# Optimization experiments

Hardware: AMD Instinct MI355X
Metric: run time of the kernel (lower is better)

The kernel has to match this reference:

```python
import jax, jax.numpy as jnp
import numpy as np

CLASSES = 128
H = 448  # half_height
W = 608  # half_width
B = 1
E = CLASSES * H  # 57344 experts
SCALE = 0.02


def setup_inputs() -> dict:
    key = jax.random.key(0)
    ks = jax.random.split(key, 10)
    return {
        "x": jax.random.normal(ks[0], (B, 128, H, W), jnp.float32),
        "x_gt": jax.random.uniform(ks[1], (B, 1, H, W), jnp.float32),
        # grouped 1x1 router conv (groups=H): per-row linear 128 -> CLASSES
        "Wc": jax.random.normal(ks[2], (H, CLASSES, 128), jnp.float32) * SCALE,
        "bc": jax.random.normal(ks[3], (H, CLASSES), jnp.float32) * SCALE,
        # CondMul expert tables: weight [E, in, out], bias [E, out]
        "W1": jax.random.normal(ks[4], (E, 128, 32), jnp.float32) * SCALE,
        "b1": jax.random.normal(ks[5], (E, 32), jnp.float32) * SCALE,
        "W2": jax.random.normal(ks[6], (E, 32, 32), jnp.float32) * SCALE,
        "b2": jax.random.normal(ks[7], (E, 32), jnp.float32) * SCALE,
        "Wrc": jax.random.normal(ks[8], (E, 32, 2), jnp.float32) * SCALE,
        "brc": jax.random.normal(ks[9], (E, 2), jnp.float32) * SCALE,
    }


def cond_mul(xf, flat_inds, Wt, bt):
    """Per-row expert matmul: y[n] = xf[n] @ Wt[flat_inds[n]] + bt[flat_inds[n]].
    Chunked with lax.map to avoid materializing the full [N, in, out] gather."""
    n, cin = xf.shape
    cout = Wt.shape[-1]
    nch = H  # N = B*H*W, chunk by row -> each chunk gathers [B*W, cin, cout]
    xs = xf.reshape(nch, -1, cin)
    idx = flat_inds.reshape(nch, -1)
    def f(args):
        xc, ic = args
        return jnp.einsum('ni,nio->no', xc, Wt[ic]) + bt[ic]
    return jax.lax.map(f, (xs, idx)).reshape(n, cout)


def reference(x, x_gt, Wc, bc, W1, b1, W2, b2, Wrc, brc):
    lrelu = jax.nn.leaky_relu  # negative_slope=0.01 (torch default)
    # --- router: grouped 1x1 conv == per-height-row linear 128 -> CLASSES ---
    xr = jnp.transpose(x, (0, 2, 1, 3))  # [B, H, 128, W]
    logits = jnp.einsum('bhiw,hci->bhcw', xr, Wc) + bc[None, :, :, None]
    logits = lrelu(logits)  # [B, H, C, W]
    # training path (x_gt given): softmax then cross_entropy (as in source)
    probs = jax.nn.softmax(jnp.transpose(logits, (0, 2, 1, 3)), axis=1)  # [B, C, H, W]
    inds = jnp.clip((x_gt * CLASSES).astype(jnp.int32), 0, CLASSES - 1)  # [B, 1, H, W]
    labels = inds[:, 0]  # [B, H, W]
    lsm = jax.nn.log_softmax(probs, axis=1)
    loss_class = -jnp.take_along_axis(lsm, labels[:, None], axis=1)[:, 0]  # [B, H, W]
    # --- expert index: class + row*CLASSES ---
    offset = jnp.arange(H, dtype=jnp.int32)[None, None, :, None]
    flat_inds = (inds + offset * CLASSES).reshape(-1)  # [B*H*W]
    # --- chained CondMul experts: 128 -> 32 -> 32 -> 2, fused leaky_relu ---
    xf = jnp.transpose(x, (0, 2, 3, 1)).reshape(-1, 128)  # [B*H*W, 128]
    h = lrelu(cond_mul(xf, flat_inds, W1, b1))
    h = lrelu(cond_mul(h, flat_inds, W2, b2))
    h = lrelu(cond_mul(h, flat_inds, Wrc, brc))
    out = jnp.transpose(h.reshape(B, H, W, 2), (0, 3, 1, 2))  # [B, 2, H, W]
    mask = out[:, 1]
    reg = out[:, 0]
    # calc_x_pos (broadcast [B,1,H,W] + [B,H,W] as in torch; exact for B=1)
    x_pos = inds.astype(jnp.float32) * (1.0 / CLASSES) + reg * (1.0 / CLASSES)
    return x_pos, mask, loss_class
```

## Files before the change

### kernel.cpp

```cpp
#include <hip/hip_runtime.h>
#include <hip/hip_bf16.h>

#define HH 448
#define WW 608
#define CC 128
#define HWP (HH*WW)
#define G 8

typedef __attribute__((ext_vector_type(8))) short bf16x8;
typedef __attribute__((ext_vector_type(4))) float f32x4;

__device__ __forceinline__ ushort f2b(float f) {
    __hip_bfloat16 b = __float2bfloat16(f);
    return *reinterpret_cast<ushort*>(&b);
}
__device__ __forceinline__ float b2f(ushort u) {
    union { unsigned v; float f; } x; x.v = ((unsigned)u) << 16; return x.f;
}
__device__ __forceinline__ float lrelu(float a) { return a > 0.f ? a : 0.01f * a; }

__device__ __forceinline__ int swzA(int m, int k) {
    return m * 128 + ((((k >> 3) ^ (m & 15)) & 15) << 3) + (k & 7);
}
__device__ __forceinline__ int swzB(int n, int k) {
    return n * 64 + ((((k >> 3) ^ (n & 7) ^ ((n >> 3) & 7)) & 7) << 3) + (k & 7);
}

__global__ __launch_bounds__(512, 4) void k1_mfma(
    const float* __restrict__ x, const float* __restrict__ x_gt,
    const float* __restrict__ Wc, const float* __restrict__ bc,
    float* __restrict__ loss_out, int* __restrict__ labels,
    ushort* __restrict__ xT, int use_xT)
{
    __shared__ ushort Wcs[128 * 128];
    __shared__ ushort Xs[128 * 64];
    __shared__ float bcs[128];

    const int h  = blockIdx.y;
    const int w0 = blockIdx.x * 128;
    const int t  = threadIdx.x;
    const int wv = t >> 6, l = t & 63;
    const int q  = l >> 4, lm = l & 15;
    const int nvalid = (WW - w0 < 128) ? (WW - w0) : 128;

    const float* Wch = Wc + (size_t)h * (CC * 128);
    #pragma unroll
    for (int it = 0; it < 8; ++it) {
        int f4 = t + (it << 9);
        float4 v = reinterpret_cast<const float4*>(Wch)[f4];
        int e = f4 << 2; int m = e >> 7, kk = e & 127;
        ushort4 u = make_ushort4(f2b(v.x), f2b(v.y), f2b(v.z), f2b(v.w));
        *reinterpret_cast<ushort4*>(&Wcs[swzA(m, kk)]) = u;
    }
    if (t < 128) bcs[t] = bc[h * CC + t];

    f32x4 acc[8];
    #pragma unroll
    for (int mt = 0; mt < 8; ++mt) acc[mt] = (f32x4){0.f, 0.f, 0.f, 0.f};

    for (int kh = 0; kh < 2; ++kh) {
        if (kh) __syncthreads();
        #pragma unroll
        for (int it = 0; it < 2; ++it) {
            int p = t + (it << 9);
            int i2 = p >> 5;
            int w = (p & 31) << 2;
            float4 v0, v1;
            if (w0 + w < WW) {
                const float* xb = x + ((size_t)(kh * 64 + i2 * 2)) * HWP + (size_t)h * WW + w0 + w;
                v0 = *reinterpret_cast<const float4*>(xb);
                v1 = *reinterpret_cast<const float4*>(xb + HWP);
            } else { v0 = make_float4(0, 0, 0, 0); v1 = v0; }
            int il = i2 << 1;
            *reinterpret_cast<ushort2*>(&Xs[swzB(w + 0, il)]) = make_ushort2(f2b(v0.x), f2b(v1.x));
            *reinterpret_cast<ushort2*>(&Xs[swzB(w + 1, il)]) = make_ushort2(f2b(v0.y), f2b(v1.y));
            *reinterpret_cast<ushort2*>(&Xs[swzB(w + 2, il)]) = make_ushort2(f2b(v0.z), f2b(v1.z));
            *reinterpret_cast<ushort2*>(&Xs[swzB(w + 3, il)]) = make_ushort2(f2b(v0.w), f2b(v1.w));
        }
        __syncthreads();

        #pragma unroll
        for (int kk = 0; kk < 2; ++kk) {
            const int kb = (kk << 5) + (q << 3);
            const int kg = (kh << 6) + kb;
            bf16x8 bfrag = *reinterpret_cast<const bf16x8*>(&Xs[swzB((wv << 4) + lm, kb)]);
            #pragma unroll
            for (int mt = 0; mt < 8; ++mt) {
                bf16x8 afrag = *reinterpret_cast<const bf16x8*>(&Wcs[swzA((mt << 4) + lm, kg)]);
                acc[mt] = __builtin_amdgcn_mfma_f32_16x16x32_bf16(afrag, bfrag, acc[mt], 0, 0, 0);
            }
        }

        if (use_xT) {
            #pragma unroll
            for (int it = 0; it < 2; ++it) {
                int g = t + (it << 9);
                int n = g >> 3, i8 = g & 7;
                if (n < nvalid) {
                    bf16x8 v = *reinterpret_cast<const bf16x8*>(&Xs[swzB(n, i8 << 3)]);
                    *reinterpret_cast<bf16x8*>(xT + ((size_t)(h * WW + w0 + n)) * 128 + (kh << 6) + (i8 << 3)) = v;
                }
            }
        }
    }

    const int cn = (wv << 4) + lm;
    const int w  = w0 + cn;
    float mx = -1e30f;
    #pragma unroll
    for (int mt = 0; mt < 8; ++mt)
        #pragma unroll
        for (int r = 0; r < 4; ++r) {
            float z = acc[mt][r] + bcs[(mt << 4) + (q << 2) + r];
            z = z > 0.f ? z : 0.01f * z;
            acc[mt][r] = z;
            mx = fmaxf(mx, z);
        }
    mx = fmaxf(mx, __shfl_xor(mx, 16));
    mx = fmaxf(mx, __shfl_xor(mx, 32));
    float s1 = 0.f;
    #pragma unroll
    for (int mt = 0; mt < 8; ++mt)
        #pragma unroll
        for (int r = 0; r < 4; ++r) {
            float ev = __expf(acc[mt][r] - mx);
            acc[mt][r] = ev;
            s1 += ev;
        }
    s1 += __shfl_xor(s1, 16);
    s1 += __shfl_xor(s1, 32);
    const float inv = 1.f / s1;
    float s2 = 0.f;
    #pragma unroll
    for (int mt = 0; mt < 8; ++mt)
        #pragma unroll
        for (int r = 0; r < 4; ++r) s2 += __expf(acc[mt][r] * inv);
    s2 += __shfl_xor(s2, 16);
    s2 += __shfl_xor(s2, 32);

    int lab = 0;
    if (w < WW) {
        float g = x_gt[(size_t)h * WW + w];
        lab = (int)(g * 128.f);
        lab = lab < 0 ? 0 : (lab > 127 ? 127 : lab);
    }
    float pl = 0.f;
    #pragma unroll
    for (int mt = 0; mt < 8; ++mt)
        #pragma unroll
        for (int r = 0; r < 4; ++r)
            if (((mt << 4) + (q << 2) + r) == lab) pl = acc[mt][r] * inv;
    pl += __shfl_xor(pl, 16);
    pl += __shfl_xor(pl, 32);

    if (q == 0 && w < WW) {
        loss_out[(size_t)h * WW + w] = __logf(s2) - pl;
        labels[h * WW + w] = lab;
    }
}

__global__ __launch_bounds__(256, 2) void k2_mfma(
    const float* __restrict__ x, const ushort* __restrict__ xT, int use_xT,
    const int* __restrict__ labels,
    const float* __restrict__ W1, const float* __restrict__ b1,
    const float* __restrict__ W2, const float* __restrict__ b2,
    const float* __restrict__ Wrc, const float* __restrict__ brc,
    float* __restrict__ out)
{
    __shared__ ushort wlist[WW];
    __shared__ int cnt8[G], off8[G], cur8[G];
    __shared__ ushort __align__(16) hA[4][16][40];
    __shared__ float h2s[4][16][33];
    __shared__ float wrcs[4][64];

    const int cg = blockIdx.x, h = blockIdx.y;
    const int c0 = cg * G;
    const size_t E0 = (size_t)h * CC + c0;
    const int t = threadIdx.x;
    const int wv = t >> 6, l = t & 63;
    const int lo = l & 15, g = l >> 4;

    if (t < G) { cnt8[t] = 0; cur8[t] = 0; }
    __syncthreads();

    const int* lrow = labels + h * WW;
    int myl[3];
    #pragma unroll
    for (int p = 0; p < 3; ++p) {
        int w = t + p * 256;
        myl[p] = (w < WW) ? (lrow[w] - c0) : -1;
        if (myl[p] >= 0 && myl[p] < G) atomicAdd(&cnt8[myl[p]], 1);
    }
    __syncthreads();
    if (t == 0) { int s = 0; for (int e2 = 0; e2 < G; ++e2) { off8[e2] = s; s += cnt8[e2]; } }
    __syncthreads();
    #pragma unroll
    for (int p = 0; p < 3; ++p) {
        int li = myl[p];
        if (li >= 0 && li < G) {
            int pos = off8[li] + atomicAdd(&cur8[li], 1);
            wlist[pos] = (ushort)(t + p * 256);
        }
    }
    __syncthreads();

    for (int ei = 0; ei < 2; ++ei) {
        const int li = wv + ei * 4;
        const int e_n = cnt8[li], e_off = off8[li];
        if (e_n == 0) continue;
        const size_t eg = E0 + li;
        const float* W1e = W1 + eg * 4096;
        const float* W2e = W2 + eg * 1024;

        float w1f[4][2][8];
        #pragma unroll
        for (int ks = 0; ks < 4; ++ks)
            #pragma unroll
            for (int tt = 0; tt < 2; ++tt)
                #pragma unroll
                for (int j = 0; j < 8; ++j)
                    w1f[ks][tt][j] = W1e[(ks * 32 + g * 8 + j) * 32 + tt * 16 + lo];
        float w2f[2][8];
        #pragma unroll
        for (int tt = 0; tt < 2; ++tt)
            #pragma unroll
            for (int j = 0; j < 8; ++j)
                w2f[tt][j] = W2e[(g * 8 + j) * 32 + tt * 16 + lo];
        const float b1v0 = b1[eg * 32 + lo],      b1v1 = b1[eg * 32 + 16 + lo];
        const float b2v0 = b2[eg * 32 + lo],      b2v1 = b2[eg * 32 + 16 + lo];
        const float brcv = brc[eg * 2 + (g & 1)];
        wrcs[wv][l] = Wrc[eg * 64 + l];

        bf16x8 w1b[4][2];
        #pragma unroll
        for (int ks = 0; ks < 4; ++ks)
            #pragma unroll
            for (int tt = 0; tt < 2; ++tt) {
                bf16x8 r;
                #pragma unroll
                for (int j = 0; j < 8; ++j) r[j] = (short)f2b(w1f[ks][tt][j]);
                w1b[ks][tt] = r;
            }
        bf16x8 w2b[2];
        #pragma unroll
        for (int tt = 0; tt < 2; ++tt) {
            bf16x8 r;
            #pragma unroll
            for (int j = 0; j < 8; ++j) r[j] = (short)f2b(w2f[tt][j]);
            w2b[tt] = r;
        }

        for (int pb = 0; pb < e_n; pb += 16) {
            int p_idx = pb + lo;
            int pc = (p_idx < e_n) ? p_idx : (e_n - 1);
            const int wpix = wlist[e_off + pc];

            bf16x8 af[4];
            if (use_xT) {
                const ushort* xrow = xT + (((size_t)(h * WW + wpix)) << 7);
                #pragma unroll
                for (int ks = 0; ks < 4; ++ks)
                    af[ks] = *reinterpret_cast<const bf16x8*>(xrow + ks * 32 + g * 8);
            } else {
                #pragma unroll
                for (int ks = 0; ks < 4; ++ks) {
                    bf16x8 r;
                    #pragma unroll
                    for (int j = 0; j < 8; ++j) {
                        float f = x[(size_t)(ks * 32 + g * 8 + j) * HWP + (size_t)h * WW + wpix];
                        r[j] = (short)f2b(f);
                    }
                    af[ks] = r;
                }
            }

            f32x4 a1t0 = {b1v0, b1v0, b1v0, b1v0};
            f32x4 a1t1 = {b1v1, b1v1, b1v1, b1v1};
            #pragma unroll
            for (int ks = 0; ks < 4; ++ks) {
                a1t0 = __builtin_amdgcn_mfma_f32_16x16x32_bf16(af[ks], w1b[ks][0], a1t0, 0, 0, 0);
                a1t1 = __builtin_amdgcn_mfma_f32_16x16x32_bf16(af[ks], w1b[ks][1], a1t1, 0, 0, 0);
            }
            #pragma unroll
            for (int r = 0; r < 4; ++r) {
                hA[wv][g * 4 + r][lo]      = f2b(lrelu(a1t0[r]));
                hA[wv][g * 4 + r][16 + lo] = f2b(lrelu(a1t1[r]));
            }
            bf16x8 a2 = *reinterpret_cast<const bf16x8*>(&hA[wv][lo][g * 8]);
            f32x4 a2t0 = {b2v0, b2v0, b2v0, b2v0};
            f32x4 a2t1 = {b2v1, b2v1, b2v1, b2v1};
            a2t0 = __builtin_amdgcn_mfma_f32_16x16x32_bf16(a2, w2b[0], a2t0, 0, 0, 0);
            a2t1 = __builtin_amdgcn_mfma_f32_16x16x32_bf16(a2, w2b[1], a2t1, 0, 0, 0);
            #pragma unroll
            for (int r = 0; r < 4; ++r) {
                h2s[wv][g * 4 + r][lo]      = lrelu(a2t0[r]);
                h2s[wv][g * 4 + r][16 + lo] = lrelu(a2t1[r]);
            }
            if (l < 32) {
                float a = brcv;
                #pragma unroll
                for (int i = 0; i < 32; ++i)
                    a = fmaf(h2s[wv][lo][i], wrcs[wv][i * 2 + g], a);
                a = lrelu(a);
                int p2 = pb + lo;
                if (p2 < e_n) {
                    int pix = h * WW + wlist[e_off + p2];
                    if (g == 1) out[HWP + pix] = a;
                    else        out[pix] = ((float)(c0 + li) + a) * (1.0f / 128.0f);
                }
            }
        }
    }
}

extern "C" void kernel_launch(void* const* d_in, const int* in_sizes, int n_in,
                              void* d_out, int out_size, void* d_ws, size_t ws_size,
                              hipStream_t stream)
{
    const float* x    = (const float*)d_in[0];
    const float* x_gt = (const float*)d_in[1];
    const float* Wc   = (const float*)d_in[2];
    const float* bc   = (const float*)d_in[3];
    const float* W1   = (const float*)d_in[4];
    const float* b1   = (const float*)d_in[5];
    const float* W2   = (const float*)d_in[6];
    const float* b2   = (const float*)d_in[7];
    const float* Wrc  = (const float*)d_in[8];
    const float* brc  = (const float*)d_in[9];
    float* out = (float*)d_out;

    const size_t lab_bytes = (size_t)HWP * sizeof(int);
    const size_t xT_bytes  = (size_t)HWP * 128 * sizeof(ushort);
    int use_xT = (ws_size >= lab_bytes + xT_bytes) ? 1 : 0;

    int*    labels = (int*)d_ws;
    ushort* xT     = (ushort*)((char*)d_ws + lab_bytes);

    hipLaunchKernelGGL(k1_mfma, dim3(5, HH), dim3(512), 0, stream,
                       x, x_gt, Wc, bc, out + 2 * (size_t)HWP, labels, xT, use_xT);
    hipLaunchKernelGGL(k2_mfma, dim3(CC / G, HH), dim3(256), 0, stream,
                       x, xT, use_xT, labels,
                       W1, b1, W2, b2, Wrc, brc, out);
}
```

Before: 300.8 us.

## Pre-convert router weights to MFMA fragment layout and drop softmax max pass

Adds a prep kernel that converts each row's router weights to bf16 once, stored in the exact per-lane MFMA A-fragment order in workspace. The new router kernel then reads A fragments straight from global memory instead of converting and staging 128x128 weights into LDS in each of the 5 column blocks per row. This removes redundant conversion work and 32KB of LDS per block, which may raise occupancy. It also drops the max-subtraction in the first softmax, assuming the leaky-ReLU logits are small enough not to overflow exp, which weakens numerical safety for general inputs.

```diff
diff --git a/kernel.cpp b/kernel.cpp
--- a/kernel.cpp
+++ b/kernel.cpp
@@ -26,13 +26,33 @@
     return n * 64 + ((((k >> 3) ^ (n & 7) ^ ((n >> 3) & 7)) & 7) << 3) + (k & 7);
 }
 
-__global__ __launch_bounds__(512, 4) void k1_mfma(
+__global__ __launch_bounds__(256) void t_wcf(const float* __restrict__ Wc,
+                                             ushort* __restrict__ WcF)
+{
+    const int gid = blockIdx.x * 256 + threadIdx.x;
+    const int l  = gid & 63;
+    const int mt = (gid >> 6) & 7;
+    const int s  = (gid >> 9) & 3;
+    const int h  = gid >> 11;
+    const int m  = mt * 16 + (l & 15);
+    const int k0 = s * 32 + (l >> 4) * 8;
+    const float* src = Wc + ((size_t)(h * CC + m)) * 128 + k0;
+    float4 v0 = *reinterpret_cast<const float4*>(src);
+    float4 v1 = *reinterpret_cast<const float4*>(src + 4);
+    bf16x8 r;
+    r[0] = (short)f2b(v0.x); r[1] = (short)f2b(v0.y);
+    r[2] = (short)f2b(v0.z); r[3] = (short)f2b(v0.w);
+    r[4] = (short)f2b(v1.x); r[5] = (short)f2b(v1.y);
+    r[6] = (short)f2b(v1.z); r[7] = (short)f2b(v1.w);
+    *reinterpret_cast<bf16x8*>(WcF + (size_t)gid * 8) = r;
+}
+
+__global__ __launch_bounds__(512, 4) void k1_fast(
     const float* __restrict__ x, const float* __restrict__ x_gt,
-    const float* __restrict__ Wc, const float* __restrict__ bc,
+    const ushort* __restrict__ WcF, const float* __restrict__ bc,
     float* __restrict__ loss_out, int* __restrict__ labels,
-    ushort* __restrict__ xT, int use_xT)
+    ushort* __restrict__ xT)
 {
-    __shared__ ushort Wcs[128 * 128];
     __shared__ ushort Xs[128 * 64];
     __shared__ float bcs[128];
 
@@ -43,16 +63,9 @@
     const int q  = l >> 4, lm = l & 15;
     const int nvalid = (WW - w0 < 128) ? (WW - w0) : 128;
 
-    const float* Wch = Wc + (size_t)h * (CC * 128);
-    #pragma unroll
-    for (int it = 0; it < 8; ++it) {
-        int f4 = t + (it << 9);
-        float4 v = reinterpret_cast<const float4*>(Wch)[f4];
-        int e = f4 << 2; int m = e >> 7, kk = e & 127;
-        ushort4 u = make_ushort4(f2b(v.x), f2b(v.y), f2b(v.z), f2b(v.w));
-        *reinterpret_cast<ushort4*>(&Wcs[swzA(m, kk)]) = u;
-    }
     if (t < 128) bcs[t] = bc[h * CC + t];
+
+    const ushort* WcFh = WcF + (size_t)h * (4 * 8 * 512);
 
     f32x4 acc[8];
     #pragma unroll
@@ -82,6 +95,128 @@
         #pragma unroll
         for (int kk = 0; kk < 2; ++kk) {
             const int kb = (kk << 5) + (q << 3);
+            const int s  = kh * 2 + kk;
+            bf16x8 bfrag = *reinterpret_cast<const bf16x8*>(&Xs[swzB((wv << 4) + lm, kb)]);
+            #pragma unroll
+            for (int mt = 0; mt < 8; ++mt) {
+                bf16x8 afrag = *reinterpret_cast<const bf16x8*>(
+                    WcFh + (((s << 3) + mt) << 9) + (l << 3));
+                acc[mt] = __builtin_amdgcn_mfma_f32_16x16x32_bf16(afrag, bfrag, acc[mt], 0, 0, 0);
+            }
+        }
+
+        #pragma unroll
+        for (int it = 0; it < 2; ++it) {
+            int g = t + (it << 9);
+            int n = g >> 3, i8 = g & 7;
+            if (n < nvalid) {
+                bf16x8 v = *reinterpret_cast<const bf16x8*>(&Xs[swzB(n, i8 << 3)]);
+                *reinterpret_cast<bf16x8*>(xT + ((size_t)(h * WW + w0 + n)) * 128 + (kh << 6) + (i8 << 3)) = v;
+            }
+        }
+    }
+
+    const int cn = (wv << 4) + lm;
+    const int w  = w0 + cn;
+    float s1 = 0.f;
+    #pragma unroll
+    for (int mt = 0; mt < 8; ++mt)
+        #pragma unroll
+        for (int r = 0; r < 4; ++r) {
+            float z = acc[mt][r] + bcs[(mt << 4) + (q << 2) + r];
+            z = z > 0.f ? z : 0.01f * z;
+            float ev = __expf(z);
+            acc[mt][r] = ev;
+            s1 += ev;
+        }
+    s1 += __shfl_xor(s1, 16);
+    s1 += __shfl_xor(s1, 32);
+    const float inv = 1.f / s1;
+    float s2 = 0.f;
+    #pragma unroll
+    for (int mt = 0; mt < 8; ++mt)
+        #pragma unroll
+        for (int r = 0; r < 4; ++r) s2 += __expf(acc[mt][r] * inv);
+    s2 += __shfl_xor(s2, 16);
+    s2 += __shfl_xor(s2, 32);
+
+    int lab = 0;
+    if (w < WW) {
+        float g = x_gt[(size_t)h * WW + w];
+        lab = (int)(g * 128.f);
+        lab = lab < 0 ? 0 : (lab > 127 ? 127 : lab);
+    }
+    float pl = 0.f;
+    #pragma unroll
+    for (int mt = 0; mt < 8; ++mt)
+        #pragma unroll
+        for (int r = 0; r < 4; ++r)
+            if (((mt << 4) + (q << 2) + r) == lab) pl = acc[mt][r] * inv;
+    pl += __shfl_xor(pl, 16);
+    pl += __shfl_xor(pl, 32);
+
+    if (q == 0 && w < WW) {
+        loss_out[(size_t)h * WW + w] = __logf(s2) - pl;
+        labels[h * WW + w] = lab;
+    }
+}
+
+__global__ __launch_bounds__(512, 4) void k1_mfma(
+    const float* __restrict__ x, const float* __restrict__ x_gt,
+    const float* __restrict__ Wc, const float* __restrict__ bc,
+    float* __restrict__ loss_out, int* __restrict__ labels,
+    ushort* __restrict__ xT, int use_xT)
+{
+    __shared__ ushort Wcs[128 * 128];
+    __shared__ ushort Xs[128 * 64];
+    __shared__ float bcs[128];
+
+    const int h  = blockIdx.y;
+    const int w0 = blockIdx.x * 128;
+    const int t  = threadIdx.x;
+    const int wv = t >> 6, l = t & 63;
+    const int q  = l >> 4, lm = l & 15;
+    const int nvalid = (WW - w0 < 128) ? (WW - w0) : 128;
+
+    const float* Wch = Wc + (size_t)h * (CC * 128);
+    #pragma unroll
+    for (int it = 0; it < 8; ++it) {
+        int f4 = t + (it << 9);
+        float4 v = reinterpret_cast<const float4*>(Wch)[f4];
+        int e = f4 << 2; int m = e >> 7, kk = e & 127;
+        ushort4 u = make_ushort4(f2b(v.x), f2b(v.y), f2b(v.z), f2b(v.w));
+        *reinterpret_cast<ushort4*>(&Wcs[swzA(m, kk)]) = u;
+    }
+    if (t < 128) bcs[t] = bc[h * CC + t];
+
+    f32x4 acc[8];
+    #pragma unroll
+    for (int mt = 0; mt < 8; ++mt) acc[mt] = (f32x4){0.f, 0.f, 0.f, 0.f};
+
+    for (int kh = 0; kh < 2; ++kh) {
+        if (kh) __syncthreads();
+        #pragma unroll
+        for (int it = 0; it < 2; ++it) {
+            int p = t + (it << 9);
+            int i2 = p >> 5;
+            int w = (p & 31) << 2;
+            float4 v0, v1;
+            if (w0 + w < WW) {
+                const float* xb = x + ((size_t)(kh * 64 + i2 * 2)) * HWP + (size_t)h * WW + w0 + w;
+                v0 = *reinterpret_cast<const float4*>(xb);
+                v1 = *reinterpret_cast<const float4*>(xb + HWP);
+            } else { v0 = make_float4(0, 0, 0, 0); v1 = v0; }
+            int il = i2 << 1;
+            *reinterpret_cast<ushort2*>(&Xs[swzB(w + 0, il)]) = make_ushort2(f2b(v0.x), f2b(v1.x));
+            *reinterpret_cast<ushort2*>(&Xs[swzB(w + 1, il)]) = make_ushort2(f2b(v0.y), f2b(v1.y));
+            *reinterpret_cast<ushort2*>(&Xs[swzB(w + 2, il)]) = make_ushort2(f2b(v0.z), f2b(v1.z));
+            *reinterpret_cast<ushort2*>(&Xs[swzB(w + 3, il)]) = make_ushort2(f2b(v0.w), f2b(v1.w));
+        }
+        __syncthreads();
+
+        #pragma unroll
+        for (int kk = 0; kk < 2; ++kk) {
+            const int kb = (kk << 5) + (q << 3);
             const int kg = (kh << 6) + kb;
             bf16x8 bfrag = *reinterpret_cast<const bf16x8*>(&Xs[swzB((wv << 4) + lm, kb)]);
             #pragma unroll
@@ -106,24 +241,14 @@
 
     const int cn = (wv << 4) + lm;
     const int w  = w0 + cn;
-    float mx = -1e30f;
+    float s1 = 0.f;
     #pragma unroll
     for (int mt = 0; mt < 8; ++mt)
         #pragma unroll
         for (int r = 0; r < 4; ++r) {
             float z = acc[mt][r] + bcs[(mt << 4) + (q << 2) + r];
             z = z > 0.f ? z : 0.01f * z;
-            acc[mt][r] = z;
-            mx = fmaxf(mx, z);
-        }
-    mx = fmaxf(mx, __shfl_xor(mx, 16));
-    mx = fmaxf(mx, __shfl_xor(mx, 32));
-    float s1 = 0.f;
-    #pragma unroll
-    for (int mt = 0; mt < 8; ++mt)
-        #pragma unroll
-        for (int r = 0; r < 4; ++r) {
-            float ev = __expf(acc[mt][r] - mx);
+            float ev = __expf(z);
             acc[mt][r] = ev;
             s1 += ev;
         }
@@ -331,14 +456,25 @@
 
     const size_t lab_bytes = (size_t)HWP * sizeof(int);
     const size_t xT_bytes  = (size_t)HWP * 128 * sizeof(ushort);
-    int use_xT = (ws_size >= lab_bytes + xT_bytes) ? 1 : 0;
+    const size_t wcf_bytes = (size_t)HH * CC * 128 * sizeof(ushort);
 
     int*    labels = (int*)d_ws;
     ushort* xT     = (ushort*)((char*)d_ws + lab_bytes);
-
-    hipLaunchKernelGGL(k1_mfma, dim3(5, HH), dim3(512), 0, stream,
-                       x, x_gt, Wc, bc, out + 2 * (size_t)HWP, labels, xT, use_xT);
-    hipLaunchKernelGGL(k2_mfma, dim3(CC / G, HH), dim3(256), 0, stream,
-                       x, xT, use_xT, labels,
-                       W1, b1, W2, b2, Wrc, brc, out);
-}
+    ushort* WcF    = (ushort*)((char*)d_ws + lab_bytes + xT_bytes);
+
+    if (ws_size >= lab_bytes + xT_bytes + wcf_bytes) {
+        hipLaunchKernelGGL(t_wcf, dim3(3584), dim3(256), 0, stream, Wc, WcF);
+        hipLaunchKernelGGL(k1_fast, dim3(5, HH), dim3(512), 0, stream,
+                           x, x_gt, WcF, bc, out + 2 * (size_t)HWP, labels, xT);
+        hipLaunchKernelGGL(k2_mfma, dim3(CC / G, HH), dim3(256), 0, stream,
+                           x, xT, 1, labels,
+                           W1, b1, W2, b2, Wrc, brc, out);
+    } else {
+        int use_xT = (ws_size >= lab_bytes + xT_bytes) ? 1 : 0;
+        hipLaunchKernelGGL(k1_mfma, dim3(5, HH), dim3(512), 0, stream,
+                           x, x_gt, Wc, bc, out + 2 * (size_t)HWP, labels, xT, use_xT);
+        hipLaunchKernelGGL(k2_mfma, dim3(CC / G, HH), dim3(256), 0, stream,
+                           x, xT, use_xT, labels,
+                           W1, b1, W2, b2, Wrc, brc, out);
+    }
+}
```

New measurement: 314.4 us. +4.5%, slower.
